# Kernel optimization log

Measured on AMD Instinct MI355X. Metric: run time of the kernel, lower is better.

## Reference

```python
import jax, jax.numpy as jnp
import numpy as np

B, N, CZ, CH, CA, H, TN = 1, 256, 128, 128, 32, 4, 4


def setup_inputs() -> dict:
    key = jax.random.key(0)
    ks = iter(jax.random.split(key, 64))

    def rn(shape, s=0.02):
        return jax.random.normal(next(ks), shape, dtype=jnp.float32) * s

    d = {"z": jax.random.normal(next(ks), (B, N, N, CZ), dtype=jnp.float32)}
    # Triangle multiplication params, stacked [2, ...]: idx 0 = outgoing, 1 = incoming
    d["tm_ln_in_w"] = jnp.ones((2, CZ)); d["tm_ln_in_b"] = jnp.zeros((2, CZ))
    for nm, shp in [("ap", (2, CZ, CH)), ("ag", (2, CZ, CH)), ("bp", (2, CZ, CH)),
                    ("bg", (2, CZ, CH)), ("g", (2, CZ, CZ)), ("zo", (2, CH, CZ))]:
        d[f"tm_{nm}_w"] = rn(shp)
        d[f"tm_{nm}_b"] = jnp.zeros((2, shp[-1]))
    d["tm_lnout_w"] = jnp.ones((2, CH)); d["tm_lnout_b"] = jnp.zeros((2, CH))
    # Triangle attention params, stacked [2, ...]: idx 0 = start, 1 = end
    d["ta_ln_w"] = jnp.ones((2, CZ)); d["ta_ln_b"] = jnp.zeros((2, CZ))
    d["ta_q_w"] = rn((2, CZ, H * CA)); d["ta_k_w"] = rn((2, CZ, H * CA)); d["ta_v_w"] = rn((2, CZ, H * CA))
    d["ta_b_w"] = rn((2, CZ, H))
    d["ta_g_w"] = rn((2, CZ, H * CA)); d["ta_g_b"] = jnp.zeros((2, H * CA))
    d["ta_o_w"] = rn((2, H * CA, CZ)); d["ta_o_b"] = jnp.zeros((2, CZ))
    # Pair transition
    d["pt_ln_w"] = jnp.ones((CZ,)); d["pt_ln_b"] = jnp.zeros((CZ,))
    d["pt_1_w"] = rn((CZ, TN * CZ)); d["pt_1_b"] = jnp.zeros((TN * CZ,))
    d["pt_2_w"] = rn((TN * CZ, CZ)); d["pt_2_b"] = jnp.zeros((CZ,))
    return d


def _ln(x, w, b, eps=1e-5):
    m = jnp.mean(x, axis=-1, keepdims=True)
    v = jnp.mean(jnp.square(x - m), axis=-1, keepdims=True)
    return (x - m) * jax.lax.rsqrt(v + eps) * w + b


def _tri_mul(z, lnw, lnb, apw, apb, agw, agb, bpw, bpb, bgw, bgb, gw, gb,
             lnow, lnob, zw, zb, outgoing):
    x = _ln(z, lnw, lnb)
    a = jax.nn.sigmoid(x @ agw + agb) * (x @ apw + apb)  # [B,I,J,CH]
    b = jax.nn.sigmoid(x @ bgw + bgb) * (x @ bpw + bpb)
    eq = 'bikc,bjkc->bijc' if outgoing else 'bkic,bkjc->bijc'
    t = jnp.einsum(eq, a, b)  # O(N^3 * CH)
    t = _ln(t, lnow, lnob) @ zw + zb
    return t * jax.nn.sigmoid(x @ gw + gb)


def _tri_att(z, lnw, lnb, qw, kw, vw, bw, gw, gb, ow, ob):
    Bz, I, J, _ = z.shape
    x = _ln(z, lnw, lnb)
    # triangle bias [B,1,H,I,J] (broadcast over query row)
    bias = jnp.einsum('bijc,ch->bhij', x, bw)[:, None]
    q = (x @ qw).reshape(Bz, I, J, H, CA).transpose(0, 1, 3, 2, 4) / np.float32(np.sqrt(CA))
    k = (x @ kw).reshape(Bz, I, J, H, CA).transpose(0, 1, 3, 2, 4)
    v = (x @ vw).reshape(Bz, I, J, H, CA).transpose(0, 1, 3, 2, 4)
    a = jnp.einsum('bihqc,bihkc->bihqk', q, k) + bias  # [B,I,H,J,J]
    p = jax.nn.softmax(a, axis=-1)
    o = jnp.einsum('bihqk,bihkc->bihqc', p, v).transpose(0, 1, 3, 2, 4).reshape(Bz, I, J, H * CA)
    o = o * jax.nn.sigmoid(x @ gw + gb)
    return o @ ow + ob


def reference(z, tm_ln_in_w, tm_ln_in_b, tm_ap_w, tm_ap_b, tm_ag_w, tm_ag_b,
              tm_bp_w, tm_bp_b, tm_bg_w, tm_bg_b, tm_g_w, tm_g_b,
              tm_lnout_w, tm_lnout_b, tm_zo_w, tm_zo_b,
              ta_ln_w, ta_ln_b, ta_q_w, ta_k_w, ta_v_w, ta_b_w,
              ta_g_w, ta_g_b, ta_o_w, ta_o_b,
              pt_ln_w, pt_ln_b, pt_1_w, pt_1_b, pt_2_w, pt_2_b):
    def tm(zz, i, outgoing):
        return _tri_mul(zz, tm_ln_in_w[i], tm_ln_in_b[i], tm_ap_w[i], tm_ap_b[i],
                        tm_ag_w[i], tm_ag_b[i], tm_bp_w[i], tm_bp_b[i],
                        tm_bg_w[i], tm_bg_b[i], tm_g_w[i], tm_g_b[i],
                        tm_lnout_w[i], tm_lnout_b[i], tm_zo_w[i], tm_zo_b[i], outgoing)

    def ta(zz, i):
        return _tri_att(zz, ta_ln_w[i], ta_ln_b[i], ta_q_w[i], ta_k_w[i], ta_v_w[i],
                        ta_b_w[i], ta_g_w[i], ta_g_b[i], ta_o_w[i], ta_o_b[i])

    z = z + tm(z, 0, True)          # triangle mult outgoing + residual (dropout = eval identity)
    z = z + tm(z, 1, False)         # triangle mult incoming + residual
    z = z + ta(z, 0)                # triangle attention (starting node)
    zt = jnp.swapaxes(z, 1, 2)      # transpose for ending-node attention
    zt = zt + ta(zt, 1)
    z = jnp.swapaxes(zt, 1, 2)
    x = _ln(z, pt_ln_w, pt_ln_b)    # pair transition
    z = z + (jax.nn.relu(x @ pt_1_w + pt_1_b) @ pt_2_w + pt_2_b)
    return z
```

## Files before the change

kernel.cpp:

```cpp
#include <hip/hip_runtime.h>
#include <math.h>

#define N_  256
#define NN  65536
#define CZ  128
#define CH  128
#define H_  4
#define CA  32

typedef __attribute__((ext_vector_type(8))) short bf16x8;
typedef __attribute__((ext_vector_type(4))) float f32x4;

__device__ __forceinline__ float sigmoidf_(float x){ return 1.f/(1.f+__expf(-x)); }

__device__ __forceinline__ short f2b(float f){
  unsigned u = __float_as_uint(f);
  unsigned r = (u + 0x7fffu + ((u>>16)&1u)) >> 16;
  return (short)r;
}
__device__ __forceinline__ float b2f(short s){
  unsigned u = ((unsigned)(unsigned short)s) << 16;
  return __uint_as_float(u);
}
__device__ __forceinline__ unsigned pk_bf16(float lo, float hi){
  unsigned r;
  asm volatile("v_cvt_pk_bf16_f32 %0, %1, %2" : "=v"(r) : "v"(lo), "v"(hi));
  return r;
}

__device__ __forceinline__ void glds16(const void* g, const void* l){
  __builtin_amdgcn_global_load_lds((const __attribute__((address_space(1))) void*)g,
                                   (__attribute__((address_space(3))) void*)l, 16, 0, 0);
}

__device__ __forceinline__ float wave_red_sum(float v){
  #pragma unroll
  for(int o=32;o>0;o>>=1) v += __shfl_xor(v,o,64);
  return v;
}

__device__ __forceinline__ int Gperm(int t, int m){
  return ((t>>1)<<5) + ((m>>2)<<3) + ((t&1)<<2) + (m&3);
}

__global__ void __launch_bounds__(256) prep_weights(
    const float* tm_ag, const float* tm_ap, const float* tm_bg, const float* tm_bp,
    const float* tm_g, const float* tm_zo,
    const float* ta_q, const float* ta_k, const float* ta_v, const float* ta_g, const float* ta_o,
    const float* pt1, const float* pt2, short* Wf){
  int tid = threadIdx.x;
  int g = blockIdx.x*4 + (tid>>6);
  int l = tid & 63;
  int s = blockIdx.y;
  const float* src; int ldn = 128, koff = 0, noff = 0;
  if (s < 12){
    int i = s/6, w = s - i*6;
    switch(w){ case 0: src=tm_ag; break; case 1: src=tm_ap; break; case 2: src=tm_bg; break;
               case 3: src=tm_bp; break; case 4: src=tm_g;  break; default: src=tm_zo; }
    src += i*16384;
  } else if (s < 22){
    int t2 = s-12; int i = t2/5, w = t2 - i*5;
    switch(w){ case 0: src=ta_q; break; case 1: src=ta_k; break; case 2: src=ta_v; break;
               case 3: src=ta_g; break; default: src=ta_o; }
    src += i*16384;
  } else if (s < 26){
    src = pt1; ldn = 512; noff = (s-22)*128;
  } else {
    src = pt2; koff = (s-26)*128;
  }
  int nt = g>>2, ks = g&3;
  int n = noff + nt*16 + (l&15);
  int kb = koff + ks*32 + (l>>4)*8;
  short tmp[8];
  #pragma unroll
  for (int e=0;e<8;e++) tmp[e] = f2b(src[(size_t)(kb+e)*ldn + n]);
  short* dst = Wf + s*16384 + ((nt*4+ks)*64 + l)*8;
  *(short4*)dst     = *(short4*)&tmp[0];
  *(short4*)(dst+4) = *(short4*)&tmp[4];
}

template<bool TRANS>
__global__ void __launch_bounds__(256) ln_x(const float* __restrict__ in,
                                            const float* __restrict__ w,
                                            const float* __restrict__ b,
                                            short* __restrict__ out){
  int wid  = threadIdx.x >> 6;
  int lane = threadIdx.x & 63;
  int row  = blockIdx.x*4 + wid;
  int irow;
  if (TRANS){ int i = row >> 8, j = row & 255; irow = (j<<8) | i; } else irow = row;
  float v0 = in[(size_t)irow*CZ + lane];
  float v1 = in[(size_t)irow*CZ + lane + 64];
  float m  = wave_red_sum(v0+v1) * (1.f/128.f);
  float d0 = v0-m, d1 = v1-m;
  float var = wave_red_sum(d0*d0 + d1*d1) * (1.f/128.f);
  float r = rsqrtf(var + 1e-5f);
  out[(size_t)row*CZ + lane]      = f2b(d0*r*w[lane]    + b[lane]);
  out[(size_t)row*CZ + lane + 64] = f2b(d1*r*w[lane+64] + b[lane+64]);
}

__device__ __forceinline__ void stage128(const short* __restrict__ g, short* xs, int r0, int tid){
  #pragma unroll
  for (int m=0;m<8;++m){
    int d = m*256 + tid;
    int row = d>>4, cw = d&15;
    glds16(&g[(size_t)(r0+row)*128 + ((cw ^ (row&15))<<3)], xs + (size_t)(d & ~63)*8);
  }
}

__device__ __forceinline__ bf16x8 ldsA(const short* xs, int row, int ch){
  return *(const bf16x8*)&xs[row*128 + ((ch ^ (row&15))<<3)];
}

__device__ __forceinline__ void gemm_core(const short* xs, const short* __restrict__ wf,
                                          int wm, int wn, int l, f32x4 (&acc)[4][4]){
  #pragma unroll
  for (int ks=0; ks<4; ++ks){
    bf16x8 a[4], b[4];
    #pragma unroll
    for (int mt=0; mt<4; ++mt)
      a[mt] = ldsA(xs, wm*64 + mt*16 + (l&15), ks*4 + (l>>4));
    #pragma unroll
    for (int nt=0; nt<4; ++nt)
      b[nt] = *(const bf16x8*)&wf[(((wn*4+nt)*4 + ks)*64 + l)*8];
    #pragma unroll
    for (int mt=0; mt<4; ++mt)
      #pragma unroll
      for (int nt=0; nt<4; ++nt)
        acc[mt][nt] = __builtin_amdgcn_mfma_f32_16x16x32_bf16(a[mt], b[nt], acc[mt][nt], 0,0,0);
  }
}

__device__ __forceinline__ void gemm_core2(const short* xs, const short* __restrict__ wf1,
                                           const short* __restrict__ wf2,
                                           int wm, int wn, int l,
                                           f32x4 (&acc1)[4][4], f32x4 (&acc2)[4][4]){
  #pragma unroll
  for (int ks=0; ks<4; ++ks){
    bf16x8 a[4], b1[4], b2[4];
    #pragma unroll
    for (int mt=0; mt<4; ++mt)
      a[mt] = ldsA(xs, wm*64 + mt*16 + (l&15), ks*4 + (l>>4));
    #pragma unroll
    for (int nt=0; nt<4; ++nt){
      b1[nt] = *(const bf16x8*)&wf1[(((wn*4+nt)*4 + ks)*64 + l)*8];
      b2[nt] = *(const bf16x8*)&wf2[(((wn*4+nt)*4 + ks)*64 + l)*8];
    }
    #pragma unroll
    for (int mt=0; mt<4; ++mt)
      #pragma unroll
      for (int nt=0; nt<4; ++nt){
        acc1[mt][nt] = __builtin_amdgcn_mfma_f32_16x16x32_bf16(a[mt], b1[nt], acc1[mt][nt], 0,0,0);
        acc2[mt][nt] = __builtin_amdgcn_mfma_f32_16x16x32_bf16(a[mt], b2[nt], acc2[mt][nt], 0,0,0);
      }
  }
}

#define GEMM_PROLOG \
  int tid = threadIdx.x; int r0 = blockIdx.x*128; \
  int wid = tid>>6, l = tid&63; int wm = wid>>1, wn = wid&1;

#define EPI_COORDS \
  int row = wm*64 + mt*16 + ((l>>4)<<2) + reg; \
  int col = wn*64 + nt*16 + (l&15);

__global__ void __launch_bounds__(256) k_dual_gate(const short* __restrict__ X,
                                                   const short* __restrict__ Wgf, const float* __restrict__ bg,
                                                   const short* __restrict__ Wpf, const float* __restrict__ bp,
                                                   short* __restrict__ out){
  __shared__ short xs[128*128];
  GEMM_PROLOG
  stage128(X, xs, r0, tid);
  __syncthreads();
  f32x4 ag[4][4], ap[4][4];
  #pragma unroll
  for(int a=0;a<4;a++) for(int b=0;b<4;b++){ ag[a][b]=(f32x4){0,0,0,0}; ap[a][b]=(f32x4){0,0,0,0}; }
  gemm_core2(xs, Wgf, Wpf, wm, wn, l, ag, ap);
  #pragma unroll
  for (int mt=0; mt<4; ++mt)
    #pragma unroll
    for (int nt=0; nt<4; ++nt)
      #pragma unroll
      for (int reg=0; reg<4; ++reg){
        EPI_COORDS
        float v = (ap[mt][nt][reg] + bp[col]) * sigmoidf_(ag[mt][nt][reg] + bg[col]);
        out[(size_t)(r0+row)*128 + col] = f2b(v);
      }
}

__global__ void __launch_bounds__(256) k_dual_scale(const short* __restrict__ X,
                                                    const short* __restrict__ W1f, float s1,
                                                    const short* __restrict__ W2f, float s2,
                                                    short* __restrict__ out1, short* __restrict__ out2){
  __shared__ short xs[128*128];
  GEMM_PROLOG
  stage128(X, xs, r0, tid);
  __syncthreads();
  f32x4 a1[4][4], a2[4][4];
  #pragma unroll
  for(int a=0;a<4;a++) for(int b=0;b<4;b++){ a1[a][b]=(f32x4){0,0,0,0}; a2[a][b]=(f32x4){0,0,0,0}; }
  gemm_core2(xs, W1f, W2f, wm, wn, l, a1, a2);
  #pragma unroll
  for (int mt=0; mt<4; ++mt)
    #pragma unroll
    for (int nt=0; nt<4; ++nt)
      #pragma unroll
      for (int reg=0; reg<4; ++reg){
        EPI_COORDS
        out1[(size_t)(r0+row)*128 + col] = f2b(a1[mt][nt][reg]*s1);
        out2[(size_t)(r0+row)*128 + col] = f2b(a2[mt][nt][reg]*s2);
      }
}

__global__ void __launch_bounds__(256) k_gemm_t(const short* __restrict__ X,
                                                const short* __restrict__ Wf,
                                                short* __restrict__ Vt){
  __shared__ short xs[128*128];
  __shared__ short tt[128*132];
  GEMM_PROLOG
  stage128(X, xs, r0, tid);
  __syncthreads();
  f32x4 acc[4][4];
  #pragma unroll
  for(int a=0;a<4;a++) for(int b=0;b<4;b++) acc[a][b]=(f32x4){0,0,0,0};
  gemm_core(xs, Wf, wm, wn, l, acc);
  #pragma unroll
  for (int mt=0; mt<4; ++mt)
    #pragma unroll
    for (int nt=0; nt<4; ++nt)
      #pragma unroll
      for (int reg=0; reg<4; reg+=2){
        int row = wm*64 + mt*16 + ((l>>4)<<2) + reg;
        int col = wn*64 + nt*16 + (l&15);
        short2 p = { f2b(acc[mt][nt][reg]), f2b(acc[mt][nt][reg+1]) };
        *(short2*)&tt[col*132 + row] = p;
      }
  __syncthreads();
  int i = r0>>8, j0 = r0&255;
  #pragma unroll
  for (int m=0;m<8;++m){
    int idx = m*256 + tid;
    int c = idx>>4, ch = idx&15;
    int4 val = *(const int4*)&tt[c*132 + ch*8];
    *(int4*)&Vt[(size_t)((i*4 + (c>>5))*32 + (c&31))*256 + j0 + ch*8] = val;
  }
}

__global__ void __launch_bounds__(256) k_tri_finish(const short* __restrict__ T2,
                                                    const short* __restrict__ X,
                                                    const short* __restrict__ Wzf, const float* __restrict__ bz,
                                                    const short* __restrict__ Wgf, const float* __restrict__ bg,
                                                    const float* __restrict__ zin, float* __restrict__ zout){
  __shared__ short ts[128*128];
  __shared__ short xs[128*128];
  GEMM_PROLOG
  stage128(T2, ts, r0, tid);
  stage128(X,  xs, r0, tid);
  __syncthreads();
  f32x4 az[4][4], ag[4][4];
  #pragma unroll
  for(int a=0;a<4;a++) for(int b=0;b<4;b++){ az[a][b]=(f32x4){0,0,0,0}; ag[a][b]=(f32x4){0,0,0,0}; }
  gemm_core(ts, Wzf, wm, wn, l, az);
  gemm_core(xs, Wgf, wm, wn, l, ag);
  #pragma unroll
  for (int mt=0; mt<4; ++mt)
    #pragma unroll
    for (int nt=0; nt<4; ++nt)
      #pragma unroll
      for (int reg=0; reg<4; ++reg){
        EPI_COORDS
        size_t idx = (size_t)(r0+row)*128 + col;
        float v = (az[mt][nt][reg] + bz[col]) * sigmoidf_(ag[mt][nt][reg] + bg[col]);
        zout[idx] = zin[idx] + v;
      }
}

template<bool TRANS>
__global__ void __launch_bounds__(256) k_attn_out(const short* __restrict__ O,
                                                  const short* __restrict__ X,
                                                  const short* __restrict__ Wgf, const float* __restrict__ bg,
                                                  const short* __restrict__ Wof, const float* __restrict__ bo,
                                                  float* __restrict__ z){
  __shared__ short xs[128*128];
  __shared__ short os[128*128];
  GEMM_PROLOG
  stage128(X, xs, r0, tid);
  #pragma unroll
  for (int m=0;m<8;++m){
    int d = m*256 + tid;
    int row = d>>4, ch = d&15;
    glds16(&O[(size_t)(r0+row)*128 + ch*8], os + (size_t)(d & ~63)*8);
  }
  __syncthreads();
  f32x4 ag[4][4];
  #pragma unroll
  for(int a=0;a<4;a++) for(int b=0;b<4;b++) ag[a][b]=(f32x4){0,0,0,0};
  gemm_core(xs, Wgf, wm, wn, l, ag);
  __syncthreads();
  #pragma unroll
  for (int mt=0; mt<4; ++mt)
    #pragma unroll
    for (int nt=0; nt<4; ++nt)
      #pragma unroll
      for (int reg=0; reg<4; ++reg){
        EPI_COORDS
        float ov = b2f(os[row*128 + col]);
        float v = ov * sigmoidf_(ag[mt][nt][reg] + bg[col]);
        xs[row*128 + (((col>>3) ^ (row&15))<<3) + (col&7)] = f2b(v);
      }
  __syncthreads();
  f32x4 a2[4][4];
  #pragma unroll
  for(int a=0;a<4;a++) for(int b=0;b<4;b++) a2[a][b]=(f32x4){0,0,0,0};
  gemm_core(xs, Wof, wm, wn, l, a2);
  #pragma unroll
  for (int mt=0; mt<4; ++mt)
    #pragma unroll
    for (int nt=0; nt<4; ++nt)
      #pragma unroll
      for (int reg=0; reg<4; ++reg){
        EPI_COORDS
        int orow = r0+row;
        int zrow = TRANS ? (((orow&255)<<8) | (orow>>8)) : orow;
        z[(size_t)zrow*128 + col] += a2[mt][nt][reg] + bo[col];
      }
}

__global__ void __launch_bounds__(256) k_pt(const short* __restrict__ X,
                                            const short* __restrict__ W1f, const float* __restrict__ b1,
                                            const short* __restrict__ W2f, const float* __restrict__ b2,
                                            float* __restrict__ z){
  __shared__ short xs[128*128];
  __shared__ short hs[128*128];
  GEMM_PROLOG
  stage128(X, xs, r0, tid);
  __syncthreads();
  f32x4 a2[4][4];
  #pragma unroll
  for(int a=0;a<4;a++) for(int b=0;b<4;b++) a2[a][b]=(f32x4){0,0,0,0};
  for (int m=0;m<4;++m){
    f32x4 a1[4][4];
    #pragma unroll
    for(int a=0;a<4;a++) for(int b=0;b<4;b++) a1[a][b]=(f32x4){0,0,0,0};
    gemm_core(xs, W1f + m*16384, wm, wn, l, a1);
    #pragma unroll
    for (int mt=0; mt<4; ++mt)
      #pragma unroll
      for (int nt=0; nt<4; ++nt)
        #pragma unroll
        for (int reg=0; reg<4; ++reg){
          EPI_COORDS
          float v = fmaxf(a1[mt][nt][reg] + b1[m*128 + col], 0.f);
          hs[row*128 + (((col>>3) ^ (row&15))<<3) + (col&7)] = f2b(v);
        }
    __syncthreads();
    gemm_core(hs, W2f + m*16384, wm, wn, l, a2);
    __syncthreads();
  }
  #pragma unroll
  for (int mt=0; mt<4; ++mt)
    #pragma unroll
    for (int nt=0; nt<4; ++nt)
      #pragma unroll
      for (int reg=0; reg<4; ++reg){
        EPI_COORDS
        z[(size_t)(r0+row)*128 + col] += a2[mt][nt][reg] + b2[col];
      }
}

template<bool TR>
__global__ void __launch_bounds__(256) pack_cxy(const short* __restrict__ inA, const short* __restrict__ inB,
                                                short* __restrict__ outA, short* __restrict__ outB){
  __shared__ short tile[256*144];
  const short* in = blockIdx.y ? inB : inA;
  short* out      = blockIdx.y ? outB : outA;
  int x = blockIdx.x, tid = threadIdx.x;
  #pragma unroll
  for (int m=0;m<16;++m){
    int idx = m*256 + tid;
    int y = idx>>4, c0 = (idx&15)*8;
    int r = TR ? (y*256 + x) : (x*256 + y);
    *(int4*)&tile[y*144 + c0] = *(const int4*)&in[(size_t)r*128 + c0];
  }
  __syncthreads();
  int c = tid & 127, yh = tid >> 7;
  short* ob = out + (size_t)c*65536 + x*256 + yh*128;
  #pragma unroll
  for (int yc=0; yc<16; ++yc){
    short tmp[8];
    #pragma unroll
    for (int e=0;e<8;e++) tmp[e] = tile[(yh*128 + yc*8 + e)*144 + c];
    *(int4*)&ob[yc*8] = *(int4*)tmp;
  }
}

__global__ void __launch_bounds__(256) k_einsum(const short* __restrict__ Ab,
                                                const short* __restrict__ Bb,
                                                float* __restrict__ Tt){
  __shared__ short as[128*64];
  __shared__ short bs[128*64];
  int c = blockIdx.z;
  int i0 = blockIdx.x*128, j0 = blockIdx.y*128;
  const short* A = Ab + (size_t)c*65536;
  const short* B = Bb + (size_t)c*65536;
  int tid = threadIdx.x;
  int wid = tid>>6, l = tid&63; int wm = wid>>1, wn = wid&1;
  f32x4 acc[4][4];
  #pragma unroll
  for(int a=0;a<4;a++) for(int b=0;b<4;b++) acc[a][b]=(f32x4){0,0,0,0};
  for (int kt=0; kt<4; ++kt){
    __syncthreads();
    #pragma unroll
    for (int m=0;m<4;++m){
      int d = m*256 + tid;
      int row = d>>3, cw = d&7;
      glds16(&A[(size_t)(i0+row)*256 + kt*64 + ((cw ^ (row&7))<<3)], as + (size_t)(d & ~63)*8);
      glds16(&B[(size_t)(j0+row)*256 + kt*64 + ((cw ^ (row&7))<<3)], bs + (size_t)(d & ~63)*8);
    }
    __syncthreads();
    #pragma unroll
    for (int ks=0; ks<2; ++ks){
      bf16x8 a[4], b[4];
      #pragma unroll
      for (int mt=0; mt<4; ++mt){
        int row = wm*64 + mt*16 + (l&15);
        int ch  = (ks*4 + (l>>4)) ^ (row&7);
        a[mt] = *(const bf16x8*)&as[row*64 + ch*8];
      }
      #pragma unroll
      for (int nt=0; nt<4; ++nt){
        int row = wn*64 + nt*16 + (l&15);
        int ch  = (ks*4 + (l>>4)) ^ (row&7);
        b[nt] = *(const bf16x8*)&bs[row*64 + ch*8];
      }
      #pragma unroll
      for (int mt=0; mt<4; ++mt)
        #pragma unroll
        for (int nt=0; nt<4; ++nt)
          acc[mt][nt] = __builtin_amdgcn_mfma_f32_16x16x32_bf16(a[mt], b[nt], acc[mt][nt], 0,0,0);
    }
  }
  float* To = Tt + (size_t)c*65536;
  #pragma unroll
  for (int mt=0; mt<4; ++mt)
    #pragma unroll
    for (int nt=0; nt<4; ++nt)
      #pragma unroll
      for (int reg=0; reg<4; ++reg){
        int row = wm*64 + mt*16 + ((l>>4)<<2) + reg;
        int col = wn*64 + nt*16 + (l&15);
        To[(size_t)(i0+row)*256 + j0+col] = acc[mt][nt][reg];
      }
}

__global__ void __launch_bounds__(256) ln_t(const float* __restrict__ Tt,
                                            const float* __restrict__ w,
                                            const float* __restrict__ b,
                                            short* __restrict__ out){
  __shared__ float tile[128*68];
  __shared__ float red_s[4][64], red_q[4][64];
  __shared__ float mu[64], inv[64];
  int tid = threadIdx.x;
  int r0 = blockIdx.x*64;
  for (int m=0;m<32;++m){
    int idx = m*256 + tid;
    int c = idx>>6, rl = idx&63;
    tile[c*68 + rl] = Tt[(size_t)c*65536 + r0 + rl];
  }
  __syncthreads();
  {
    int rl = tid & 63, cq = tid >> 6;
    float s = 0.f, q = 0.f;
    #pragma unroll
    for (int cc=0; cc<32; ++cc){
      float v = tile[(cq*32+cc)*68 + rl];
      s += v; q += v*v;
    }
    red_s[cq][rl] = s; red_q[cq][rl] = q;
  }
  __syncthreads();
  if (tid < 64){
    float s = red_s[0][tid]+red_s[1][tid]+red_s[2][tid]+red_s[3][tid];
    float q = red_q[0][tid]+red_q[1][tid]+red_q[2][tid]+red_q[3][tid];
    float m = s * (1.f/128.f);
    float var = q * (1.f/128.f) - m*m;
    mu[tid] = m; inv[tid] = rsqrtf(var + 1e-5f);
  }
  __syncthreads();
  {
    int rl = tid >> 2, cq = tid & 3;
    float m = mu[rl], iv = inv[rl];
    #pragma unroll
    for (int i=0;i<32;++i){
      int cc = cq*32 + i;
      float v = (tile[cc*68 + rl] - m) * iv * w[cc] + b[cc];
      out[(size_t)(r0+rl)*128 + cc] = f2b(v);
    }
  }
}

__global__ void __launch_bounds__(256) bias_gemm(const short* __restrict__ X,
                                                 const float* __restrict__ bw,
                                                 float* __restrict__ BSF){
  __shared__ float xs[64][129];
  int r0 = blockIdx.x*64;
  for(int idx=threadIdx.x; idx<64*128; idx+=256)
    xs[idx>>7][idx&127] = b2f(X[(size_t)(r0+(idx>>7))*CZ + (idx&127)]);
  __syncthreads();
  int h = threadIdx.x>>6, r = threadIdx.x&63;
  float acc=0.f;
  #pragma unroll 4
  for(int k=0;k<CZ;k++) acc += xs[r][k]*bw[k*H_+h];
  int rr2 = r0 + r;
  int q = rr2 >> 8, j = rr2 & 255;
  int t = ((j>>5)<<1) + ((j>>2)&1);
  int m = (((j>>3)&3)<<2) + (j&3);
  int idx = (((h*16 + (q>>4))*16 + t) << 8) + (((m>>2)*16 + (q&15)) << 2) + (m&3);
  BSF[idx] = acc;
}

__global__ void __launch_bounds__(256, 3) attn_mfma(const short* __restrict__ Qg,
                                                    const short* __restrict__ Kg,
                                                    const short* __restrict__ Vt,
                                                    const float* __restrict__ BSF,
                                                    short* __restrict__ O){
  __shared__ short Kf[8192];
  __shared__ short Vf[8192];
  int i = blockIdx.x, h = blockIdx.y;
  int tid = threadIdx.x;
  #pragma unroll
  for (int m=0;m<4;++m){
    int d = m*256 + tid;
    int t = d>>6, ll = d&63;
    glds16(&Kg[(size_t)(i*N_ + Gperm(t, ll&15))*CH + h*CA + ((ll>>4)<<3)],
           Kf + (size_t)(d & ~63)*8);
    glds16(&Vt[(size_t)(((i*H_ + h)*CA) + ((t>>3)<<4) + (ll&15))*N_ + ((t&7)<<5) + ((ll>>4)<<3)],
           Vf + (size_t)(d & ~63)*8);
  }
  __syncthreads();

  int wid = tid >> 6, l = tid & 63;
  int lg = l >> 4, ln = l & 15;

  for (int ss=0; ss<4; ++ss){
    int sub = wid*4 + ss;
    bf16x8 qfrag = *(const bf16x8*)&Qg[(size_t)(i*N_ + sub*16 + ln)*CH + h*CA + (lg<<3)];
    const float* bb = BSF + (size_t)(h*16 + sub)*4096 + (l<<2);
    f32x4 acc[16];
    #pragma unroll
    for (int t=0;t<16;t++) acc[t] = *(const f32x4*)&bb[t<<8];
    #pragma unroll
    for (int t=0;t<16;t++){
      bf16x8 kf = *(const bf16x8*)&Kf[t*512 + l*8];
      acc[t] = __builtin_amdgcn_mfma_f32_16x16x32_bf16(kf, qfrag, acc[t], 0,0,0);
    }
    float mx = -1e30f;
    #pragma unroll
    for (int t=0;t<16;t++)
      mx = fmaxf(mx, fmaxf(fmaxf(acc[t][0],acc[t][1]), fmaxf(acc[t][2],acc[t][3])));
    mx = fmaxf(mx, __shfl_xor(mx,16,64));
    mx = fmaxf(mx, __shfl_xor(mx,32,64));
    float sum = 0.f;
    #pragma unroll
    for (int t=0;t<16;t++){
      #pragma unroll
      for (int r=0;r<4;r++){ float p = __expf(acc[t][r]-mx); acc[t][r]=p; sum += p; }
    }
    sum += __shfl_xor(sum,16,64);
    sum += __shfl_xor(sum,32,64);
    float iv = 1.0f / sum;
    bf16x8 pf[8];
    #pragma unroll
    for (int jt=0;jt<8;jt++){
      int4 w4;
      w4.x = pk_bf16(acc[2*jt  ][0], acc[2*jt  ][1]);
      w4.y = pk_bf16(acc[2*jt  ][2], acc[2*jt  ][3]);
      w4.z = pk_bf16(acc[2*jt+1][0], acc[2*jt+1][1]);
      w4.w = pk_bf16(acc[2*jt+1][2], acc[2*jt+1][3]);
      pf[jt] = *(bf16x8*)&w4;
    }
    #pragma unroll
    for (int ct=0; ct<2; ++ct){
      f32x4 oe = {0.f,0.f,0.f,0.f}, oo = {0.f,0.f,0.f,0.f};
      #pragma unroll
      for (int jt=0;jt<8;jt+=2){
        bf16x8 ve = *(const bf16x8*)&Vf[((ct*8 + jt  )*64 + l)*8];
        bf16x8 vo = *(const bf16x8*)&Vf[((ct*8 + jt+1)*64 + l)*8];
        oe = __builtin_amdgcn_mfma_f32_16x16x32_bf16(ve, pf[jt  ], oe, 0,0,0);
        oo = __builtin_amdgcn_mfma_f32_16x16x32_bf16(vo, pf[jt+1], oo, 0,0,0);
      }
      int q = sub*16 + ln;
      int c = ct*16 + lg*4;
      short4 ov = { f2b((oe[0]+oo[0])*iv), f2b((oe[1]+oo[1])*iv),
                    f2b((oe[2]+oo[2])*iv), f2b((oe[3]+oo[3])*iv) };
      *(short4*)&O[(size_t)(i*N_ + q)*CH + h*CA + c] = ov;
    }
  }
}

extern "C" void kernel_launch(void* const* d_in, const int* in_sizes, int n_in,
                              void* d_out, int out_size, void* d_ws, size_t ws_size,
                              hipStream_t stream) {
  const float* z_in      = (const float*)d_in[0];
  const float* tm_lnin_w = (const float*)d_in[1];
  const float* tm_lnin_b = (const float*)d_in[2];
  const float* tm_ap_w   = (const float*)d_in[3];
  const float* tm_ap_b   = (const float*)d_in[4];
  const float* tm_ag_w   = (const float*)d_in[5];
  const float* tm_ag_b   = (const float*)d_in[6];
  const float* tm_bp_w   = (const float*)d_in[7];
  const float* tm_bp_b   = (const float*)d_in[8];
  const float* tm_bg_w   = (const float*)d_in[9];
  const float* tm_bg_b   = (const float*)d_in[10];
  const float* tm_g_w    = (const float*)d_in[11];
  const float* tm_g_b    = (const float*)d_in[12];
  const float* tm_zo_w   = (const float*)d_in[13];
  const float* tm_zo_b   = (const float*)d_in[14];
  const float* tm_lno_w  = (const float*)d_in[15];
  const float* tm_lno_b  = (const float*)d_in[16];
  const float* ta_ln_w   = (const float*)d_in[17];
  const float* ta_ln_b   = (const float*)d_in[18];
  const float* ta_q_w    = (const float*)d_in[19];
  const float* ta_k_w    = (const float*)d_in[20];
  const float* ta_v_w    = (const float*)d_in[21];
  const float* ta_b_w    = (const float*)d_in[22];
  const float* ta_g_w    = (const float*)d_in[23];
  const float* ta_g_b    = (const float*)d_in[24];
  const float* ta_o_w    = (const float*)d_in[25];
  const float* ta_o_b    = (const float*)d_in[26];
  const float* pt_ln_w   = (const float*)d_in[27];
  const float* pt_ln_b   = (const float*)d_in[28];
  const float* pt_1_w    = (const float*)d_in[29];
  const float* pt_1_b    = (const float*)d_in[30];
  const float* pt_2_w    = (const float*)d_in[31];
  const float* pt_2_b    = (const float*)d_in[32];

  float* z  = (float*)d_out;
  char* base = (char*)d_ws;
  const size_t MB = 1u<<20;
  short* wf  = (short*)base;
  short* Xb  = (short*)(base + 1*MB);
  short* R1  = (short*)(base + 17*MB);
  short* R2  = (short*)(base + 33*MB);
  short* R3  = (short*)(base + 49*MB);
  short* R4  = (short*)(base + 65*MB);
  float* Tf  = (float*)(base + 81*MB);
  float* BSF = (float*)(base + 113*MB);

  #define SL(s) (wf + (size_t)(s)*16384)

  prep_weights<<<dim3(8,30), 256, 0, stream>>>(tm_ag_w, tm_ap_w, tm_bg_w, tm_bp_w,
                                               tm_g_w, tm_zo_w,
                                               ta_q_w, ta_k_w, ta_v_w, ta_g_w, ta_o_w,
                                               pt_1_w, pt_2_w, wf);

  for (int i=0;i<2;i++){
    const float* zsrc = (i==0) ? z_in : z;
    ln_x<false><<<NN/4, 256, 0, stream>>>(zsrc, tm_lnin_w+i*CZ, tm_lnin_b+i*CZ, Xb);
    k_dual_gate<<<NN/128, 256, 0, stream>>>(Xb, SL(i*6+0), tm_ag_b+i*CH, SL(i*6+1), tm_ap_b+i*CH, R1);
    k_dual_gate<<<NN/128, 256, 0, stream>>>(Xb, SL(i*6+2), tm_bg_b+i*CH, SL(i*6+3), tm_bp_b+i*CH, R2);
    if (i==0) pack_cxy<false><<<dim3(256,2), 256, 0, stream>>>(R1, R2, R3, R4);
    else      pack_cxy<true ><<<dim3(256,2), 256, 0, stream>>>(R1, R2, R3, R4);
    k_einsum<<<dim3(2,2,128), 256, 0, stream>>>(R3, R4, Tf);
    ln_t<<<NN/64, 256, 0, stream>>>(Tf, tm_lno_w+i*CH, tm_lno_b+i*CH, R1);
    k_tri_finish<<<NN/128, 256, 0, stream>>>(R1, Xb, SL(i*6+5), tm_zo_b+i*CZ,
                                             SL(i*6+4), tm_g_b+i*CZ, zsrc, z);
  }

  for (int i=0;i<2;i++){
    if (i==0) ln_x<false><<<NN/4, 256, 0, stream>>>(z, ta_ln_w, ta_ln_b, Xb);
    else      ln_x<true ><<<NN/4, 256, 0, stream>>>(z, ta_ln_w+CZ, ta_ln_b+CZ, Xb);
    k_dual_scale<<<NN/128, 256, 0, stream>>>(Xb, SL(12+i*5+0), 0.17677669529663687f,
                                             SL(12+i*5+1), 1.f, R1, R2);
    k_gemm_t<<<NN/128, 256, 0, stream>>>(Xb, SL(12+i*5+2), R3);
    bias_gemm<<<NN/64, 256, 0, stream>>>(Xb, ta_b_w+i*CZ*H_, BSF);
    attn_mfma<<<dim3(N_,H_), 256, 0, stream>>>(R1, R2, R3, BSF, R4);
    if (i==0) k_attn_out<false><<<NN/128, 256, 0, stream>>>(R4, Xb, SL(12+i*5+3), ta_g_b+i*H_*CA,
                                                            SL(12+i*5+4), ta_o_b+i*CZ, z);
    else      k_attn_out<true ><<<NN/128, 256, 0, stream>>>(R4, Xb, SL(12+i*5+3), ta_g_b+i*H_*CA,
                                                            SL(12+i*5+4), ta_o_b+i*CZ, z);
  }

  ln_x<false><<<NN/4, 256, 0, stream>>>(z, pt_ln_w, pt_ln_b, Xb);
  k_pt<<<NN/128, 256, 0, stream>>>(Xb, SL(22), pt_1_b, SL(26), pt_2_b, z);
}
```

Baseline: 613.1 us.

## Fuse projection GEMMs, fold output LayerNorm into finish, use 8-wave blocks

Merges the two triangle-multiply gate GEMMs into one kernel and the Q/K/V projections into one kernel, so the activation tile is staged into LDS once. The einsum now writes bf16 instead of fp32, and the separate output LayerNorm kernel is folded into k_tri_finish, which normalises the transposed tile in LDS before the output GEMM. All MFMA GEMM kernels move from 4 to 8 waves per block with 32-row warp tiles. This is meant to cut launches and global traffic and to raise occupancy. The cost is rounding T to bf16 before LN and computing variance as E[x²]−m², which may lose some accuracy.

```diff
diff --git a/kernel.cpp b/kernel.cpp
--- a/kernel.cpp
+++ b/kernel.cpp
@@ -99,10 +99,10 @@
   out[(size_t)row*CZ + lane + 64] = f2b(d1*r*w[lane+64] + b[lane+64]);
 }
 
-__device__ __forceinline__ void stage128(const short* __restrict__ g, short* xs, int r0, int tid){
-  #pragma unroll
-  for (int m=0;m<8;++m){
-    int d = m*256 + tid;
+__device__ __forceinline__ void stage128_8(const short* __restrict__ g, short* xs, int r0, int tid){
+  #pragma unroll
+  for (int m=0;m<4;++m){
+    int d = m*512 + tid;
     int row = d>>4, cw = d&15;
     glds16(&g[(size_t)(r0+row)*128 + ((cw ^ (row&15))<<3)], xs + (size_t)(d & ~63)*8);
   }
@@ -112,42 +112,42 @@
   return *(const bf16x8*)&xs[row*128 + ((ch ^ (row&15))<<3)];
 }
 
-__device__ __forceinline__ void gemm_core(const short* xs, const short* __restrict__ wf,
-                                          int wm, int wn, int l, f32x4 (&acc)[4][4]){
+__device__ __forceinline__ void gemm_core8(const short* xs, const short* __restrict__ wf,
+                                           int wm, int wn, int l, f32x4 (&acc)[2][4]){
   #pragma unroll
   for (int ks=0; ks<4; ++ks){
-    bf16x8 a[4], b[4];
-    #pragma unroll
-    for (int mt=0; mt<4; ++mt)
-      a[mt] = ldsA(xs, wm*64 + mt*16 + (l&15), ks*4 + (l>>4));
+    bf16x8 a[2], b[4];
+    #pragma unroll
+    for (int mt=0; mt<2; ++mt)
+      a[mt] = ldsA(xs, wm*32 + mt*16 + (l&15), ks*4 + (l>>4));
     #pragma unroll
     for (int nt=0; nt<4; ++nt)
       b[nt] = *(const bf16x8*)&wf[(((wn*4+nt)*4 + ks)*64 + l)*8];
     #pragma unroll
-    for (int mt=0; mt<4; ++mt)
+    for (int mt=0; mt<2; ++mt)
       #pragma unroll
       for (int nt=0; nt<4; ++nt)
         acc[mt][nt] = __builtin_amdgcn_mfma_f32_16x16x32_bf16(a[mt], b[nt], acc[mt][nt], 0,0,0);
   }
 }
 
-__device__ __forceinline__ void gemm_core2(const short* xs, const short* __restrict__ wf1,
-                                           const short* __restrict__ wf2,
-                                           int wm, int wn, int l,
-                                           f32x4 (&acc1)[4][4], f32x4 (&acc2)[4][4]){
+__device__ __forceinline__ void gemm_core28(const short* xs, const short* __restrict__ wf1,
+                                            const short* __restrict__ wf2,
+                                            int wm, int wn, int l,
+                                            f32x4 (&acc1)[2][4], f32x4 (&acc2)[2][4]){
   #pragma unroll
   for (int ks=0; ks<4; ++ks){
-    bf16x8 a[4], b1[4], b2[4];
-    #pragma unroll
-    for (int mt=0; mt<4; ++mt)
-      a[mt] = ldsA(xs, wm*64 + mt*16 + (l&15), ks*4 + (l>>4));
+    bf16x8 a[2], b1[4], b2[4];
+    #pragma unroll
+    for (int mt=0; mt<2; ++mt)
+      a[mt] = ldsA(xs, wm*32 + mt*16 + (l&15), ks*4 + (l>>4));
     #pragma unroll
     for (int nt=0; nt<4; ++nt){
       b1[nt] = *(const bf16x8*)&wf1[(((wn*4+nt)*4 + ks)*64 + l)*8];
       b2[nt] = *(const bf16x8*)&wf2[(((wn*4+nt)*4 + ks)*64 + l)*8];
     }
     #pragma unroll
-    for (int mt=0; mt<4; ++mt)
+    for (int mt=0; mt<2; ++mt)
       #pragma unroll
       for (int nt=0; nt<4; ++nt){
         acc1[mt][nt] = __builtin_amdgcn_mfma_f32_16x16x32_bf16(a[mt], b1[nt], acc1[mt][nt], 0,0,0);
@@ -156,216 +156,225 @@
   }
 }
 
-#define GEMM_PROLOG \
+#define ZERO_ACC(A) { _Pragma("unroll") for(int _a=0;_a<2;_a++) _Pragma("unroll") for(int _b=0;_b<4;_b++) A[_a][_b]=(f32x4){0,0,0,0}; }
+
+#define GEMM_PROLOG8 \
   int tid = threadIdx.x; int r0 = blockIdx.x*128; \
-  int wid = tid>>6, l = tid&63; int wm = wid>>1, wn = wid&1;
-
-#define EPI_COORDS \
-  int row = wm*64 + mt*16 + ((l>>4)<<2) + reg; \
+  int wid = tid>>6, l = tid&63; int wm = wid>>1, wn = wid&1; (void)r0;
+
+#define EPI8 \
+  int row = wm*32 + mt*16 + ((l>>4)<<2) + reg; \
   int col = wn*64 + nt*16 + (l&15);
 
-__global__ void __launch_bounds__(256) k_dual_gate(const short* __restrict__ X,
-                                                   const short* __restrict__ Wgf, const float* __restrict__ bg,
-                                                   const short* __restrict__ Wpf, const float* __restrict__ bp,
-                                                   short* __restrict__ out){
+#define FOR_EPI for (int mt=0;mt<2;++mt) for (int nt=0;nt<4;++nt) for (int reg=0;reg<4;++reg)
+
+__global__ void __launch_bounds__(512) k_quad_gate(const short* __restrict__ X,
+                                                   const short* __restrict__ Wagf, const float* __restrict__ bag,
+                                                   const short* __restrict__ Wapf, const float* __restrict__ bap,
+                                                   const short* __restrict__ Wbgf, const float* __restrict__ bbg,
+                                                   const short* __restrict__ Wbpf, const float* __restrict__ bbp,
+                                                   short* __restrict__ out1, short* __restrict__ out2){
   __shared__ short xs[128*128];
-  GEMM_PROLOG
-  stage128(X, xs, r0, tid);
-  __syncthreads();
-  f32x4 ag[4][4], ap[4][4];
-  #pragma unroll
-  for(int a=0;a<4;a++) for(int b=0;b<4;b++){ ag[a][b]=(f32x4){0,0,0,0}; ap[a][b]=(f32x4){0,0,0,0}; }
-  gemm_core2(xs, Wgf, Wpf, wm, wn, l, ag, ap);
-  #pragma unroll
-  for (int mt=0; mt<4; ++mt)
-    #pragma unroll
-    for (int nt=0; nt<4; ++nt)
-      #pragma unroll
-      for (int reg=0; reg<4; ++reg){
-        EPI_COORDS
-        float v = (ap[mt][nt][reg] + bp[col]) * sigmoidf_(ag[mt][nt][reg] + bg[col]);
-        out[(size_t)(r0+row)*128 + col] = f2b(v);
-      }
-}
-
-__global__ void __launch_bounds__(256) k_dual_scale(const short* __restrict__ X,
-                                                    const short* __restrict__ W1f, float s1,
-                                                    const short* __restrict__ W2f, float s2,
-                                                    short* __restrict__ out1, short* __restrict__ out2){
+  GEMM_PROLOG8
+  stage128_8(X, xs, r0, tid);
+  __syncthreads();
+  {
+    f32x4 ag[2][4], ap[2][4];
+    ZERO_ACC(ag) ZERO_ACC(ap)
+    gemm_core28(xs, Wagf, Wapf, wm, wn, l, ag, ap);
+    FOR_EPI{
+      EPI8
+      float v = (ap[mt][nt][reg] + bap[col]) * sigmoidf_(ag[mt][nt][reg] + bag[col]);
+      out1[(size_t)(r0+row)*128 + col] = f2b(v);
+    }
+  }
+  {
+    f32x4 bg2[2][4], bp2[2][4];
+    ZERO_ACC(bg2) ZERO_ACC(bp2)
+    gemm_core28(xs, Wbgf, Wbpf, wm, wn, l, bg2, bp2);
+    FOR_EPI{
+      EPI8
+      float v = (bp2[mt][nt][reg] + bbp[col]) * sigmoidf_(bg2[mt][nt][reg] + bbg[col]);
+      out2[(size_t)(r0+row)*128 + col] = f2b(v);
+    }
+  }
+}
+
+__global__ void __launch_bounds__(512) k_qkv(const short* __restrict__ X,
+                                             const short* __restrict__ Wqf, float sq,
+                                             const short* __restrict__ Wkf,
+                                             const short* __restrict__ Wvf,
+                                             short* __restrict__ out_q, short* __restrict__ out_k,
+                                             short* __restrict__ Vt){
   __shared__ short xs[128*128];
-  GEMM_PROLOG
-  stage128(X, xs, r0, tid);
-  __syncthreads();
-  f32x4 a1[4][4], a2[4][4];
-  #pragma unroll
-  for(int a=0;a<4;a++) for(int b=0;b<4;b++){ a1[a][b]=(f32x4){0,0,0,0}; a2[a][b]=(f32x4){0,0,0,0}; }
-  gemm_core2(xs, W1f, W2f, wm, wn, l, a1, a2);
-  #pragma unroll
-  for (int mt=0; mt<4; ++mt)
-    #pragma unroll
-    for (int nt=0; nt<4; ++nt)
-      #pragma unroll
-      for (int reg=0; reg<4; ++reg){
-        EPI_COORDS
-        out1[(size_t)(r0+row)*128 + col] = f2b(a1[mt][nt][reg]*s1);
-        out2[(size_t)(r0+row)*128 + col] = f2b(a2[mt][nt][reg]*s2);
-      }
-}
-
-__global__ void __launch_bounds__(256) k_gemm_t(const short* __restrict__ X,
-                                                const short* __restrict__ Wf,
-                                                short* __restrict__ Vt){
-  __shared__ short xs[128*128];
-  __shared__ short tt[128*132];
-  GEMM_PROLOG
-  stage128(X, xs, r0, tid);
-  __syncthreads();
-  f32x4 acc[4][4];
-  #pragma unroll
-  for(int a=0;a<4;a++) for(int b=0;b<4;b++) acc[a][b]=(f32x4){0,0,0,0};
-  gemm_core(xs, Wf, wm, wn, l, acc);
-  #pragma unroll
-  for (int mt=0; mt<4; ++mt)
-    #pragma unroll
-    for (int nt=0; nt<4; ++nt)
-      #pragma unroll
-      for (int reg=0; reg<4; reg+=2){
-        int row = wm*64 + mt*16 + ((l>>4)<<2) + reg;
-        int col = wn*64 + nt*16 + (l&15);
-        short2 p = { f2b(acc[mt][nt][reg]), f2b(acc[mt][nt][reg+1]) };
-        *(short2*)&tt[col*132 + row] = p;
-      }
+  GEMM_PROLOG8
+  stage128_8(X, xs, r0, tid);
+  __syncthreads();
+  {
+    f32x4 aq[2][4], ak[2][4];
+    ZERO_ACC(aq) ZERO_ACC(ak)
+    gemm_core28(xs, Wqf, Wkf, wm, wn, l, aq, ak);
+    FOR_EPI{
+      EPI8
+      out_q[(size_t)(r0+row)*128 + col] = f2b(aq[mt][nt][reg]*sq);
+      out_k[(size_t)(r0+row)*128 + col] = f2b(ak[mt][nt][reg]);
+    }
+  }
+  f32x4 av[2][4];
+  ZERO_ACC(av)
+  gemm_core8(xs, Wvf, wm, wn, l, av);
+  __syncthreads();
+  #pragma unroll
+  for (int mt=0;mt<2;++mt)
+    #pragma unroll
+    for (int nt=0;nt<4;++nt){
+      int rb  = wm*32 + mt*16 + ((l>>4)<<2);
+      int col = wn*64 + nt*16 + (l&15);
+      short4 s4 = { f2b(av[mt][nt][0]), f2b(av[mt][nt][1]), f2b(av[mt][nt][2]), f2b(av[mt][nt][3]) };
+      *(short4*)&xs[col*128 + (((rb>>3) ^ (col&15))<<3) + (rb&7)] = s4;
+    }
   __syncthreads();
   int i = r0>>8, j0 = r0&255;
   #pragma unroll
-  for (int m=0;m<8;++m){
-    int idx = m*256 + tid;
-    int c = idx>>4, ch = idx&15;
-    int4 val = *(const int4*)&tt[c*132 + ch*8];
+  for (int m=0;m<4;++m){
+    int d = m*512 + tid;
+    int c = d>>4, ch = d&15;
+    int4 val = *(const int4*)&xs[c*128 + ((ch ^ (c&15))<<3)];
     *(int4*)&Vt[(size_t)((i*4 + (c>>5))*32 + (c&31))*256 + j0 + ch*8] = val;
   }
 }
 
-__global__ void __launch_bounds__(256) k_tri_finish(const short* __restrict__ T2,
+__global__ void __launch_bounds__(512) k_tri_finish(const short* __restrict__ Tb,
                                                     const short* __restrict__ X,
                                                     const short* __restrict__ Wzf, const float* __restrict__ bz,
                                                     const short* __restrict__ Wgf, const float* __restrict__ bg,
+                                                    const float* __restrict__ lnw, const float* __restrict__ lnb,
                                                     const float* __restrict__ zin, float* __restrict__ zout){
-  __shared__ short ts[128*128];
+  __shared__ short tt[128*128];
   __shared__ short xs[128*128];
-  GEMM_PROLOG
-  stage128(T2, ts, r0, tid);
-  stage128(X,  xs, r0, tid);
-  __syncthreads();
-  f32x4 az[4][4], ag[4][4];
-  #pragma unroll
-  for(int a=0;a<4;a++) for(int b=0;b<4;b++){ az[a][b]=(f32x4){0,0,0,0}; ag[a][b]=(f32x4){0,0,0,0}; }
-  gemm_core(ts, Wzf, wm, wn, l, az);
-  gemm_core(xs, Wgf, wm, wn, l, ag);
-  #pragma unroll
-  for (int mt=0; mt<4; ++mt)
-    #pragma unroll
-    for (int nt=0; nt<4; ++nt)
-      #pragma unroll
-      for (int reg=0; reg<4; ++reg){
-        EPI_COORDS
-        size_t idx = (size_t)(r0+row)*128 + col;
-        float v = (az[mt][nt][reg] + bz[col]) * sigmoidf_(ag[mt][nt][reg] + bg[col]);
-        zout[idx] = zin[idx] + v;
+  __shared__ float ps[512], pq[512];
+  __shared__ float mu[128], iv[128];
+  GEMM_PROLOG8
+  stage128_8(X, xs, r0, tid);
+  #pragma unroll
+  for (int m=0;m<4;++m){
+    int d = m*512 + tid;
+    int c = d>>4, ch = d&15;
+    glds16(&Tb[(size_t)c*65536 + r0 + ch*8], tt + (size_t)(d & ~63)*8);
+  }
+  __syncthreads();
+  int rl = tid & 127, cq = tid >> 7;
+  float vals[32]; float s = 0.f, q = 0.f;
+  #pragma unroll
+  for (int cc=0; cc<32; ++cc){
+    float v = b2f(tt[(cq*32+cc)*128 + rl]);
+    vals[cc] = v; s += v; q += v*v;
+  }
+  ps[cq*128 + rl] = s; pq[cq*128 + rl] = q;
+  __syncthreads();
+  if (tid < 128){
+    float ss = ps[tid]+ps[128+tid]+ps[256+tid]+ps[384+tid];
+    float qq = pq[tid]+pq[128+tid]+pq[256+tid]+pq[384+tid];
+    float m = ss * (1.f/128.f);
+    float var = qq * (1.f/128.f) - m*m;
+    mu[tid] = m; iv[tid] = rsqrtf(var + 1e-5f);
+  }
+  __syncthreads();
+  {
+    float m = mu[rl], r = iv[rl];
+    #pragma unroll
+    for (int chq=0; chq<4; ++chq){
+      short tmp[8];
+      #pragma unroll
+      for (int e=0;e<8;++e){
+        int cc = chq*8 + e;
+        int c = cq*32 + cc;
+        tmp[e] = f2b((vals[cc]-m)*r*lnw[c] + lnb[c]);
       }
+      int ch = cq*4 + chq;
+      *(int4*)&tt[rl*128 + ((ch ^ (rl&15))<<3)] = *(int4*)tmp;
+    }
+  }
+  __syncthreads();
+  f32x4 az[2][4], ag[2][4];
+  ZERO_ACC(az) ZERO_ACC(ag)
+  gemm_core8(tt, Wzf, wm, wn, l, az);
+  gemm_core8(xs, Wgf, wm, wn, l, ag);
+  FOR_EPI{
+    EPI8
+    size_t idx = (size_t)(r0+row)*128 + col;
+    float v = (az[mt][nt][reg] + bz[col]) * sigmoidf_(ag[mt][nt][reg] + bg[col]);
+    zout[idx] = zin[idx] + v;
+  }
 }
 
 template<bool TRANS>
-__global__ void __launch_bounds__(256) k_attn_out(const short* __restrict__ O,
+__global__ void __launch_bounds__(512) k_attn_out(const short* __restrict__ O,
                                                   const short* __restrict__ X,
                                                   const short* __restrict__ Wgf, const float* __restrict__ bg,
                                                   const short* __restrict__ Wof, const float* __restrict__ bo,
                                                   float* __restrict__ z){
   __shared__ short xs[128*128];
   __shared__ short os[128*128];
-  GEMM_PROLOG
-  stage128(X, xs, r0, tid);
-  #pragma unroll
-  for (int m=0;m<8;++m){
-    int d = m*256 + tid;
+  GEMM_PROLOG8
+  stage128_8(X, xs, r0, tid);
+  #pragma unroll
+  for (int m=0;m<4;++m){
+    int d = m*512 + tid;
     int row = d>>4, ch = d&15;
     glds16(&O[(size_t)(r0+row)*128 + ch*8], os + (size_t)(d & ~63)*8);
   }
   __syncthreads();
-  f32x4 ag[4][4];
-  #pragma unroll
-  for(int a=0;a<4;a++) for(int b=0;b<4;b++) ag[a][b]=(f32x4){0,0,0,0};
-  gemm_core(xs, Wgf, wm, wn, l, ag);
-  __syncthreads();
-  #pragma unroll
-  for (int mt=0; mt<4; ++mt)
-    #pragma unroll
-    for (int nt=0; nt<4; ++nt)
-      #pragma unroll
-      for (int reg=0; reg<4; ++reg){
-        EPI_COORDS
-        float ov = b2f(os[row*128 + col]);
-        float v = ov * sigmoidf_(ag[mt][nt][reg] + bg[col]);
-        xs[row*128 + (((col>>3) ^ (row&15))<<3) + (col&7)] = f2b(v);
-      }
-  __syncthreads();
-  f32x4 a2[4][4];
-  #pragma unroll
-  for(int a=0;a<4;a++) for(int b=0;b<4;b++) a2[a][b]=(f32x4){0,0,0,0};
-  gemm_core(xs, Wof, wm, wn, l, a2);
-  #pragma unroll
-  for (int mt=0; mt<4; ++mt)
-    #pragma unroll
-    for (int nt=0; nt<4; ++nt)
-      #pragma unroll
-      for (int reg=0; reg<4; ++reg){
-        EPI_COORDS
-        int orow = r0+row;
-        int zrow = TRANS ? (((orow&255)<<8) | (orow>>8)) : orow;
-        z[(size_t)zrow*128 + col] += a2[mt][nt][reg] + bo[col];
-      }
-}
-
-__global__ void __launch_bounds__(256) k_pt(const short* __restrict__ X,
+  f32x4 ag[2][4];
+  ZERO_ACC(ag)
+  gemm_core8(xs, Wgf, wm, wn, l, ag);
+  __syncthreads();
+  FOR_EPI{
+    EPI8
+    float ov = b2f(os[row*128 + col]);
+    float v = ov * sigmoidf_(ag[mt][nt][reg] + bg[col]);
+    xs[row*128 + (((col>>3) ^ (row&15))<<3) + (col&7)] = f2b(v);
+  }
+  __syncthreads();
+  f32x4 a2[2][4];
+  ZERO_ACC(a2)
+  gemm_core8(xs, Wof, wm, wn, l, a2);
+  FOR_EPI{
+    EPI8
+    int orow = r0+row;
+    int zrow = TRANS ? (((orow&255)<<8) | (orow>>8)) : orow;
+    z[(size_t)zrow*128 + col] += a2[mt][nt][reg] + bo[col];
+  }
+}
+
+__global__ void __launch_bounds__(512) k_pt(const short* __restrict__ X,
                                             const short* __restrict__ W1f, const float* __restrict__ b1,
                                             const short* __restrict__ W2f, const float* __restrict__ b2,
                                             float* __restrict__ z){
   __shared__ short xs[128*128];
   __shared__ short hs[128*128];
-  GEMM_PROLOG
-  stage128(X, xs, r0, tid);
-  __syncthreads();
-  f32x4 a2[4][4];
-  #pragma unroll
-  for(int a=0;a<4;a++) for(int b=0;b<4;b++) a2[a][b]=(f32x4){0,0,0,0};
+  GEMM_PROLOG8
+  stage128_8(X, xs, r0, tid);
+  __syncthreads();
+  f32x4 a2[2][4];
+  ZERO_ACC(a2)
   for (int m=0;m<4;++m){
-    f32x4 a1[4][4];
-    #pragma unroll
-    for(int a=0;a<4;a++) for(int b=0;b<4;b++) a1[a][b]=(f32x4){0,0,0,0};
-    gemm_core(xs, W1f + m*16384, wm, wn, l, a1);
-    #pragma unroll
-    for (int mt=0; mt<4; ++mt)
-      #pragma unroll
-      for (int nt=0; nt<4; ++nt)
-        #pragma unroll
-        for (int reg=0; reg<4; ++reg){
-          EPI_COORDS
-          float v = fmaxf(a1[mt][nt][reg] + b1[m*128 + col], 0.f);
-          hs[row*128 + (((col>>3) ^ (row&15))<<3) + (col&7)] = f2b(v);
-        }
+    f32x4 a1[2][4];
+    ZERO_ACC(a1)
+    gemm_core8(xs, W1f + m*16384, wm, wn, l, a1);
+    FOR_EPI{
+      EPI8
+      float v = fmaxf(a1[mt][nt][reg] + b1[m*128 + col], 0.f);
+      hs[row*128 + (((col>>3) ^ (row&15))<<3) + (col&7)] = f2b(v);
+    }
     __syncthreads();
-    gemm_core(hs, W2f + m*16384, wm, wn, l, a2);
+    gemm_core8(hs, W2f + m*16384, wm, wn, l, a2);
     __syncthreads();
   }
-  #pragma unroll
-  for (int mt=0; mt<4; ++mt)
-    #pragma unroll
-    for (int nt=0; nt<4; ++nt)
-      #pragma unroll
-      for (int reg=0; reg<4; ++reg){
-        EPI_COORDS
-        z[(size_t)(r0+row)*128 + col] += a2[mt][nt][reg] + b2[col];
-      }
+  FOR_EPI{
+    EPI8
+    z[(size_t)(r0+row)*128 + col] += a2[mt][nt][reg] + b2[col];
+  }
 }
 
 template<bool TR>
@@ -394,9 +403,9 @@
   }
 }
 
-__global__ void __launch_bounds__(256) k_einsum(const short* __restrict__ Ab,
+__global__ void __launch_bounds__(512) k_einsum(const short* __restrict__ Ab,
                                                 const short* __restrict__ Bb,
-                                                float* __restrict__ Tt){
+                                                short* __restrict__ Tb){
   __shared__ short as[128*64];
   __shared__ short bs[128*64];
   int c = blockIdx.z;
@@ -405,14 +414,13 @@
   const short* B = Bb + (size_t)c*65536;
   int tid = threadIdx.x;
   int wid = tid>>6, l = tid&63; int wm = wid>>1, wn = wid&1;
-  f32x4 acc[4][4];
-  #pragma unroll
-  for(int a=0;a<4;a++) for(int b=0;b<4;b++) acc[a][b]=(f32x4){0,0,0,0};
+  f32x4 acc[2][4];
+  ZERO_ACC(acc)
   for (int kt=0; kt<4; ++kt){
     __syncthreads();
     #pragma unroll
-    for (int m=0;m<4;++m){
-      int d = m*256 + tid;
+    for (int m=0;m<2;++m){
+      int d = m*512 + tid;
       int row = d>>3, cw = d&7;
       glds16(&A[(size_t)(i0+row)*256 + kt*64 + ((cw ^ (row&7))<<3)], as + (size_t)(d & ~63)*8);
       glds16(&B[(size_t)(j0+row)*256 + kt*64 + ((cw ^ (row&7))<<3)], bs + (size_t)(d & ~63)*8);
@@ -420,10 +428,10 @@
     __syncthreads();
     #pragma unroll
     for (int ks=0; ks<2; ++ks){
-      bf16x8 a[4], b[4];
-      #pragma unroll
-      for (int mt=0; mt<4; ++mt){
-        int row = wm*64 + mt*16 + (l&15);
+      bf16x8 a[2], b[4];
+      #pragma unroll
+      for (int mt=0; mt<2; ++mt){
+        int row = wm*32 + mt*16 + (l&15);
         int ch  = (ks*4 + (l>>4)) ^ (row&7);
         a[mt] = *(const bf16x8*)&as[row*64 + ch*8];
       }
@@ -434,68 +442,17 @@
         b[nt] = *(const bf16x8*)&bs[row*64 + ch*8];
       }
       #pragma unroll
-      for (int mt=0; mt<4; ++mt)
+      for (int mt=0; mt<2; ++mt)
         #pragma unroll
         for (int nt=0; nt<4; ++nt)
           acc[mt][nt] = __builtin_amdgcn_mfma_f32_16x16x32_bf16(a[mt], b[nt], acc[mt][nt], 0,0,0);
     }
   }
-  float* To = Tt + (size_t)c*65536;
-  #pragma unroll
-  for (int mt=0; mt<4; ++mt)
-    #pragma unroll
-    for (int nt=0; nt<4; ++nt)
-      #pragma unroll
-      for (int reg=0; reg<4; ++reg){
-        int row = wm*64 + mt*16 + ((l>>4)<<2) + reg;
-        int col = wn*64 + nt*16 + (l&15);
-        To[(size_t)(i0+row)*256 + j0+col] = acc[mt][nt][reg];
-      }
-}
-
-__global__ void __launch_bounds__(256) ln_t(const float* __restrict__ Tt,
-                                            const float* __restrict__ w,
-                                            const float* __restrict__ b,
-                                            short* __restrict__ out){
-  __shared__ float tile[128*68];
-  __shared__ float red_s[4][64], red_q[4][64];
-  __shared__ float mu[64], inv[64];
-  int tid = threadIdx.x;
-  int r0 = blockIdx.x*64;
-  for (int m=0;m<32;++m){
-    int idx = m*256 + tid;
-    int c = idx>>6, rl = idx&63;
-    tile[c*68 + rl] = Tt[(size_t)c*65536 + r0 + rl];
-  }
-  __syncthreads();
-  {
-    int rl = tid & 63, cq = tid >> 6;
-    float s = 0.f, q = 0.f;
-    #pragma unroll
-    for (int cc=0; cc<32; ++cc){
-      float v = tile[(cq*32+cc)*68 + rl];
-      s += v; q += v*v;
-    }
-    red_s[cq][rl] = s; red_q[cq][rl] = q;
-  }
-  __syncthreads();
-  if (tid < 64){
-    float s = red_s[0][tid]+red_s[1][tid]+red_s[2][tid]+red_s[3][tid];
-    float q = red_q[0][tid]+red_q[1][tid]+red_q[2][tid]+red_q[3][tid];
-    float m = s * (1.f/128.f);
-    float var = q * (1.f/128.f) - m*m;
-    mu[tid] = m; inv[tid] = rsqrtf(var + 1e-5f);
-  }
-  __syncthreads();
-  {
-    int rl = tid >> 2, cq = tid & 3;
-    float m = mu[rl], iv = inv[rl];
-    #pragma unroll
-    for (int i=0;i<32;++i){
-      int cc = cq*32 + i;
-      float v = (tile[cc*68 + rl] - m) * iv * w[cc] + b[cc];
-      out[(size_t)(r0+rl)*128 + cc] = f2b(v);
-    }
+  short* To = Tb + (size_t)c*65536;
+  FOR_EPI{
+    int row = wm*32 + mt*16 + ((l>>4)<<2) + reg;
+    int col = wn*64 + nt*16 + (l&15);
+    To[(size_t)(i0+row)*256 + j0+col] = f2b(acc[mt][nt][reg]);
   }
 }
 
@@ -644,7 +601,7 @@
   short* R2  = (short*)(base + 33*MB);
   short* R3  = (short*)(base + 49*MB);
   short* R4  = (short*)(base + 65*MB);
-  float* Tf  = (float*)(base + 81*MB);
+  short* Tb  = (short*)(base + 81*MB);
   float* BSF = (float*)(base + 113*MB);
 
   #define SL(s) (wf + (size_t)(s)*16384)
@@ -657,30 +614,30 @@
   for (int i=0;i<2;i++){
     const float* zsrc = (i==0) ? z_in : z;
     ln_x<false><<<NN/4, 256, 0, stream>>>(zsrc, tm_lnin_w+i*CZ, tm_lnin_b+i*CZ, Xb);
-    k_dual_gate<<<NN/128, 256, 0, stream>>>(Xb, SL(i*6+0), tm_ag_b+i*CH, SL(i*6+1), tm_ap_b+i*CH, R1);
-    k_dual_gate<<<NN/128, 256, 0, stream>>>(Xb, SL(i*6+2), tm_bg_b+i*CH, SL(i*6+3), tm_bp_b+i*CH, R2);
+    k_quad_gate<<<NN/128, 512, 0, stream>>>(Xb, SL(i*6+0), tm_ag_b+i*CH, SL(i*6+1), tm_ap_b+i*CH,
+                                            SL(i*6+2), tm_bg_b+i*CH, SL(i*6+3), tm_bp_b+i*CH,
+                                            R1, R2);
     if (i==0) pack_cxy<false><<<dim3(256,2), 256, 0, stream>>>(R1, R2, R3, R4);
     else      pack_cxy<true ><<<dim3(256,2), 256, 0, stream>>>(R1, R2, R3, R4);
-    k_einsum<<<dim3(2,2,128), 256, 0, stream>>>(R3, R4, Tf);
-    ln_t<<<NN/64, 256, 0, stream>>>(Tf, tm_lno_w+i*CH, tm_lno_b+i*CH, R1);
-    k_tri_finish<<<NN/128, 256, 0, stream>>>(R1, Xb, SL(i*6+5), tm_zo_b+i*CZ,
-                                             SL(i*6+4), tm_g_b+i*CZ, zsrc, z);
+    k_einsum<<<dim3(2,2,128), 512, 0, stream>>>(R3, R4, Tb);
+    k_tri_finish<<<NN/128, 512, 0, stream>>>(Tb, Xb, SL(i*6+5), tm_zo_b+i*CZ,
+                                             SL(i*6+4), tm_g_b+i*CZ,
+                                             tm_lno_w+i*CH, tm_lno_b+i*CH, zsrc, z);
   }
 
   for (int i=0;i<2;i++){
     if (i==0) ln_x<false><<<NN/4, 256, 0, stream>>>(z, ta_ln_w, ta_ln_b, Xb);
     else      ln_x<true ><<<NN/4, 256, 0, stream>>>(z, ta_ln_w+CZ, ta_ln_b+CZ, Xb);
-    k_dual_scale<<<NN/128, 256, 0, stream>>>(Xb, SL(12+i*5+0), 0.17677669529663687f,
-                                             SL(12+i*5+1), 1.f, R1, R2);
-    k_gemm_t<<<NN/128, 256, 0, stream>>>(Xb, SL(12+i*5+2), R3);
+    k_qkv<<<NN/128, 512, 0, stream>>>(Xb, SL(12+i*5+0), 0.17677669529663687f,
+                                      SL(12+i*5+1), SL(12+i*5+2), R1, R2, R3);
     bias_gemm<<<NN/64, 256, 0, stream>>>(Xb, ta_b_w+i*CZ*H_, BSF);
     attn_mfma<<<dim3(N_,H_), 256, 0, stream>>>(R1, R2, R3, BSF, R4);
-    if (i==0) k_attn_out<false><<<NN/128, 256, 0, stream>>>(R4, Xb, SL(12+i*5+3), ta_g_b+i*H_*CA,
+    if (i==0) k_attn_out<false><<<NN/128, 512, 0, stream>>>(R4, Xb, SL(12+i*5+3), ta_g_b+i*H_*CA,
                                                             SL(12+i*5+4), ta_o_b+i*CZ, z);
-    else      k_attn_out<true ><<<NN/128, 256, 0, stream>>>(R4, Xb, SL(12+i*5+3), ta_g_b+i*H_*CA,
+    else      k_attn_out<true ><<<NN/128, 512, 0, stream>>>(R4, Xb, SL(12+i*5+3), ta_g_b+i*H_*CA,
                                                             SL(12+i*5+4), ta_o_b+i*CZ, z);
   }
 
   ln_x<false><<<NN/4, 256, 0, stream>>>(z, pt_ln_w, pt_ln_b, Xb);
-  k_pt<<<NN/128, 256, 0, stream>>>(Xb, SL(22), pt_1_b, SL(26), pt_2_b, z);
-}
+  k_pt<<<NN/128, 512, 0, stream>>>(Xb, SL(22), pt_1_b, SL(26), pt_2_b, z);
+}
```

New measurement: 603.0 us. About the same (-1.7%).
